# Kernel optimization log

Hardware: AMD Instinct MI355X
Metric: run time of the kernel (lower is better)

Reference implementation:

```python
import jax, jax.numpy as jnp
import numpy as np

B, L, D = 8, 512, 128
SCALE = float(np.sqrt(D))


def setup_inputs() -> dict:
    key = jax.random.key(0)
    ks = jax.random.split(key, 12)
    s = 1.0 / np.sqrt(D)
    inp = {
        "query": jax.random.normal(ks[0], (B, L, D), jnp.float32),
        "key": jax.random.normal(ks[1], (B, L, D), jnp.float32),
        "value": jax.random.normal(ks[2], (B, L, D), jnp.float32),
        # nn.Linear weights stored torch-style as (out, in); y = x @ W.T + b
        "Wq": jax.random.uniform(ks[3], (D, D), jnp.float32, -s, s),
        "bq": jax.random.uniform(ks[4], (D,), jnp.float32, -s, s),
        "Wk": jax.random.uniform(ks[5], (D, D), jnp.float32, -s, s),
        "bk": jax.random.uniform(ks[6], (D,), jnp.float32, -s, s),
        "Wv": jax.random.uniform(ks[7], (D, D), jnp.float32, -s, s),
        "bv": jax.random.uniform(ks[8], (D,), jnp.float32, -s, s),
        "w_delta": jax.random.uniform(ks[9], (D,), jnp.float32, -s, s),
        "b_delta": jnp.zeros((), jnp.float32),
        "w_sigma": jax.random.uniform(ks[10], (D,), jnp.float32, -s, s),
        "b_sigma": jnp.zeros((), jnp.float32),
        "w_theta": jax.random.uniform(ks[11], (D,), jnp.float32, -s, s),
        "b_theta": jnp.zeros((), jnp.float32),
    }
    return inp


def reference(query, key, value, Wq, bq, Wk, bk, Wv, bv,
              w_delta, b_delta, w_sigma, b_sigma, w_theta, b_theta):
    Q = query @ Wq.T + bq          # [B,Lq,D]
    K = key @ Wk.T + bk            # [B,Lk,D]
    V = value @ Wv.T + bv          # [B,Lk,D]
    e = jnp.tanh(Q[:, :, None, :] + K[:, None, :, :])  # [B,Lq,Lk,D]
    # base (sum/scale) + three linear score heads fuse into one reduction over D
    w_all = 1.0 / SCALE + w_delta + w_sigma + w_theta   # [D]
    b_all = b_delta + b_sigma + b_theta
    combined = jnp.einsum('bqkd,d->bqk', e, w_all) + b_all
    attn = jax.nn.softmax(combined, axis=-1)            # dropout in eval mode: identity
    out = jnp.einsum('bqk,bkd->bqd', attn, V)
    return out
```

## Files before the change

kernel.cpp:

```cpp
#include <hip/hip_runtime.h>


#define BB 8
#define LL 512
#define DD 128
#define NROW (BB*LL)
#define MATN (NROW*DD)
#define KSPLIT 8

static constexpr float C1 = 2.8853900817779268f;
static constexpr float LOG2E = 1.4426950408889634f;
static constexpr float INV_SCALE = 0.08838834764831845f;

typedef float v2f __attribute__((ext_vector_type(2)));

__device__ __forceinline__ float fast_exp2(float x) { return __builtin_amdgcn_exp2f(x); }
__device__ __forceinline__ float fast_rcp(float x)  { return __builtin_amdgcn_rcpf(x); }

__device__ __forceinline__ v2f mk2(float a, float b) { v2f r; r.x = a; r.y = b; return r; }

__device__ __forceinline__ v2f fma2(v2f a, v2f b, v2f c) {
#if __has_builtin(__builtin_elementwise_fma)
    return __builtin_elementwise_fma(a, b, c);
#else
    v2f r; r.x = fmaf(a.x, b.x, c.x); r.y = fmaf(a.y, b.y, c.y); return r;
#endif
}

__device__ __forceinline__ int dperm(int c) {
    const int pmap[4] = {0, 2, 1, 3};
    return (c & ~3) | pmap[c & 3];
}

__global__ __launch_bounds__(256) void proj_kernel(
    const float* __restrict__ query, const float* __restrict__ key,
    const float* __restrict__ value,
    const float* __restrict__ Wq, const float* __restrict__ bq,
    const float* __restrict__ Wk, const float* __restrict__ bk,
    const float* __restrict__ Wv, const float* __restrict__ bv,
    const float* __restrict__ wd, const float* __restrict__ wsg,
    const float* __restrict__ wtt, float* __restrict__ ws)
{
    __shared__ __align__(16) float Wl[128 * 66];
    __shared__ __align__(16) float Xl[32 * 66];

    const int bx = blockIdx.x;
    const int m  = bx >> 7;
    const int r0 = (bx & 127) * 32;
    const float* X    = (m == 0) ? query : (m == 1) ? key : value;
    const float* W    = (m == 0) ? Wq    : (m == 1) ? Wk  : Wv;
    const float* bias = (m == 0) ? bq    : (m == 1) ? bk  : bv;
    const int t = threadIdx.x;

    if (bx == 0 && t < 128) {
        ws[(size_t)3 * MATN + dperm(t)] =
            -2.0f * LOG2E * (INV_SCALE + wd[t] + wsg[t] + wtt[t]);
    }

    const int cg = t & 31;
    const int rg = t >> 5;

    v2f acc[4][4];
    #pragma unroll
    for (int j = 0; j < 4; ++j) {
        float bj = bias[cg + 32 * j];
        #pragma unroll
        for (int i = 0; i < 4; ++i) acc[i][j] = mk2(bj, 0.f);
    }

    const float4* Wsrc = (const float4*)W;
    const float4* Xsrc = (const float4*)X;

    for (int h = 0; h < 2; ++h) {
        __syncthreads();
        #pragma unroll
        for (int j = 0; j < 8; ++j) {
            int g = t + j * 256;
            int c = g >> 4, f4 = g & 15;
            float4 v = Wsrc[c * 32 + h * 16 + f4];
            float* dst = &Wl[c * 66 + f4 * 4];
            *(float2*)dst       = make_float2(v.x, v.y);
            *(float2*)(dst + 2) = make_float2(v.z, v.w);
        }
        #pragma unroll
        for (int j = 0; j < 2; ++j) {
            int g = t + j * 256;
            int r = g >> 4, f4 = g & 15;
            float4 v = Xsrc[(r0 + r) * 32 + h * 16 + f4];
            float* dst = &Xl[r * 66 + f4 * 4];
            *(float2*)dst       = make_float2(v.x, v.y);
            *(float2*)(dst + 2) = make_float2(v.z, v.w);
        }
        __syncthreads();

        #pragma unroll 4
        for (int dg = 0; dg < 32; ++dg) {
            v2f bf[4];
            #pragma unroll
            for (int j = 0; j < 4; ++j)
                bf[j] = *(const v2f*)&Wl[(cg + 32 * j) * 66 + 2 * dg];
            v2f af[4];
            #pragma unroll
            for (int i = 0; i < 4; ++i)
                af[i] = *(const v2f*)&Xl[(rg * 4 + i) * 66 + 2 * dg];
            #pragma unroll
            for (int i = 0; i < 4; ++i)
                #pragma unroll
                for (int j = 0; j < 4; ++j)
                    acc[i][j] = fma2(af[i], bf[j], acc[i][j]);
        }
    }

    if (m == 2) {
        float* oV = ws + (size_t)2 * MATN;
        #pragma unroll
        for (int i = 0; i < 4; ++i) {
            int r = r0 + rg * 4 + i;
            #pragma unroll
            for (int j = 0; j < 4; ++j)
                oV[(size_t)r * DD + cg + 32 * j] = acc[i][j].x + acc[i][j].y;
        }
    } else {
        float* oE = ws + (size_t)m * MATN;
        const int cp = dperm(cg);
        #pragma unroll
        for (int i = 0; i < 4; ++i) {
            int r = r0 + rg * 4 + i;
            #pragma unroll
            for (int j = 0; j < 4; ++j)
                oE[(size_t)r * DD + cp + 32 * j] =
                    fast_exp2(C1 * (acc[i][j].x + acc[i][j].y));
        }
    }
}

template <bool ATOMIC>
__global__ __launch_bounds__(512, 6) void attn_kernel(
    const float* __restrict__ ws, float* __restrict__ outp,
    float* __restrict__ psump)
{
    __shared__ __align__(16) float Ekt[64 * 132];
    __shared__ __align__(16) float wl[128];
    __shared__ __align__(16) float EqL[8 * 512];

    const float* Eq  = ws;
    const float* Ek  = ws + (size_t)MATN;
    const float* Vp  = ws + (size_t)2 * MATN;

    const int bx   = blockIdx.x;
    const int qblk = bx >> 3;
    const int kx   = bx & 7;
    const int b    = qblk >> 4;
    const int wave = __builtin_amdgcn_readfirstlane((int)threadIdx.x >> 6);
    const int lane = threadIdx.x & 63;
    const int qa   = qblk * 32 + wave * 4;
    const int eqo  = wave * 512;

    {
        const float4* EqW = (const float4*)(Eq + (size_t)qa * DD);
        float4 ea = EqW[2 * lane];
        float4 eb = EqW[2 * lane + 1];
        *(float4*)&EqL[eqo + 8 * lane]     = ea;
        *(float4*)&EqL[eqo + 8 * lane + 4] = eb;
    }

    {
        const float4* sK = (const float4*)(Ek + (size_t)b * (LL * DD)
                                              + (size_t)kx * 64 * DD);
        #pragma unroll
        for (int r = 0; r < 4; ++r) {
            int g = (int)threadIdx.x + r * 512;
            int row = g >> 5, c4 = g & 31;
            *(float4*)&Ekt[row * 132 + c4 * 4] = sK[g];
        }
        if (threadIdx.x < 32)
            ((float4*)wl)[threadIdx.x] =
                ((const float4*)(ws + (size_t)3 * MATN))[threadIdx.x];
    }
    __syncthreads();

    const float* krow = &Ekt[lane * 132];
    const float4* wl4 = (const float4*)wl;
    const float* eqp  = &EqL[eqo];
    v2f S0 = mk2(0.f, 0.f), S1 = S0, S2 = S0, S3 = S0;

    #pragma unroll 2
    for (int ih = 0; ih < 16; ++ih) {
        float4 K0 = *(const float4*)(krow + 8 * ih);
        float4 K1 = *(const float4*)(krow + 8 * ih + 4);
        float4 W0 = wl4[2 * ih];
        float4 W1 = wl4[2 * ih + 1];
        v2f k0lo = mk2(K0.x, K0.y), k0hi = mk2(K0.z, K0.w);
        v2f k1lo = mk2(K1.x, K1.y), k1hi = mk2(K1.z, K1.w);
        v2f w0lo = mk2(W0.x, W0.y), w0hi = mk2(W0.z, W0.w);
        v2f w1lo = mk2(W1.x, W1.y), w1hi = mk2(W1.z, W1.w);
        #define QT(SS, QQ) { \
            float4 A0 = *(const float4*)(eqp + (QQ) * 128 + 8 * ih); \
            float4 A1 = *(const float4*)(eqp + (QQ) * 128 + 8 * ih + 4); \
            v2f X  = fma2(mk2(A0.x, A0.y), k0lo, mk2(1.f, 1.f)); \
            v2f Y  = fma2(mk2(A0.z, A0.w), k0hi, mk2(1.f, 1.f)); \
            v2f D  = X * Y;                        \
            v2f N  = fma2(w0lo, Y, w0hi * X);      \
            v2f NU = N * mk2(D.y, D.x); \
            float rr = fast_rcp(D.x * D.y); \
            SS = fma2(NU, mk2(rr, rr), SS); \
            v2f X1  = fma2(mk2(A1.x, A1.y), k1lo, mk2(1.f, 1.f)); \
            v2f Y1  = fma2(mk2(A1.z, A1.w), k1hi, mk2(1.f, 1.f)); \
            v2f D1  = X1 * Y1; \
            v2f N1  = fma2(w1lo, Y1, w1hi * X1); \
            v2f NU1 = N1 * mk2(D1.y, D1.x); \
            float rr1 = fast_rcp(D1.x * D1.y); \
            SS = fma2(NU1, mk2(rr1, rr1), SS); }
        QT(S0, 0) QT(S1, 1) QT(S2, 2) QT(S3, 3)
        #undef QT
    }
    float p0 = fast_exp2(S0.x + S0.y);
    float p1 = fast_exp2(S1.x + S1.y);
    float p2 = fast_exp2(S2.x + S2.y);
    float p3 = fast_exp2(S3.x + S3.y);

    float t0 = p0, t1 = p1, t2 = p2, t3 = p3;
    #pragma unroll
    for (int off = 32; off; off >>= 1) {
        t0 += __shfl_xor(t0, off);
        t1 += __shfl_xor(t1, off);
        t2 += __shfl_xor(t2, off);
        t3 += __shfl_xor(t3, off);
    }
    if (lane == 0) {
        if (ATOMIC) {
            atomicAdd(&psump[qa + 0], t0);
            atomicAdd(&psump[qa + 1], t1);
            atomicAdd(&psump[qa + 2], t2);
            atomicAdd(&psump[qa + 3], t3);
        } else {
            float* pp = psump + (size_t)kx * NROW + qa;
            pp[0] = t0; pp[1] = t1; pp[2] = t2; pp[3] = t3;
        }
    }

    *(float4*)&EqL[eqo + 4 * lane] = make_float4(p0, p1, p2, p3);

    const v2f* __restrict__ Vg =
        (const v2f*)(Vp + (size_t)b * (LL * DD) + (size_t)kx * 64 * DD);
    v2f o[4];
    #pragma unroll
    for (int qq = 0; qq < 4; ++qq) o[qq] = mk2(0.f, 0.f);

    #pragma unroll
    for (int g = 0; g < 8; ++g) {
        v2f v[8];
        #pragma unroll
        for (int e = 0; e < 8; ++e)
            v[e] = Vg[(size_t)(8 * g + e) * 64 + lane];
        #pragma unroll
        for (int e = 0; e < 8; ++e) {
            int kidx = 8 * g + e;
            float4 pw = *(const float4*)&EqL[eqo + 4 * kidx];
            o[0] = fma2(mk2(pw.x, pw.x), v[e], o[0]);
            o[1] = fma2(mk2(pw.y, pw.y), v[e], o[1]);
            o[2] = fma2(mk2(pw.z, pw.z), v[e], o[2]);
            o[3] = fma2(mk2(pw.w, pw.w), v[e], o[3]);
        }
    }

    const int d2 = 2 * lane;
    if (ATOMIC) {
        #pragma unroll
        for (int qq = 0; qq < 4; ++qq) {
            atomicAdd(&outp[(size_t)(qa + qq) * DD + d2],     o[qq].x);
            atomicAdd(&outp[(size_t)(qa + qq) * DD + d2 + 1], o[qq].y);
        }
    } else {
        float* base = outp + (size_t)kx * MATN;
        #pragma unroll
        for (int qq = 0; qq < 4; ++qq)
            *(v2f*)&base[(size_t)(qa + qq) * DD + d2] = o[qq];
    }
}

__global__ __launch_bounds__(256) void reduce_kernel(
    const float* __restrict__ part, const float* __restrict__ psumP,
    float* __restrict__ out)
{
    int t = blockIdx.x * 256 + threadIdx.x;
    const float4* p4 = (const float4*)part;
    float4 acc = make_float4(0.f, 0.f, 0.f, 0.f);
    #pragma unroll
    for (int kx = 0; kx < KSPLIT; ++kx) {
        float4 v = p4[(size_t)kx * (MATN / 4) + t];
        acc.x += v.x; acc.y += v.y; acc.z += v.z; acc.w += v.w;
    }
    int q = t >> 5;
    float s = 0.f;
    #pragma unroll
    for (int kx = 0; kx < KSPLIT; ++kx) s += psumP[(size_t)kx * NROW + q];
    float inv = fast_rcp(s);
    ((float4*)out)[t] = make_float4(acc.x * inv, acc.y * inv,
                                    acc.z * inv, acc.w * inv);
}

__global__ __launch_bounds__(256) void norm_kernel(
    float* __restrict__ out, const float* __restrict__ psumG)
{
    int t = blockIdx.x * 256 + threadIdx.x;
    float2* o2 = (float2*)out;
    int q = t >> 6;
    float inv = fast_rcp(psumG[q]);
    float2 v = o2[t];
    o2[t] = make_float2(v.x * inv, v.y * inv);
}

extern "C" void kernel_launch(void* const* d_in, const int* in_sizes, int n_in,
                              void* d_out, int out_size, void* d_ws, size_t ws_size,
                              hipStream_t stream) {
    const float* query = (const float*)d_in[0];
    const float* key_  = (const float*)d_in[1];
    const float* value = (const float*)d_in[2];
    const float* Wq    = (const float*)d_in[3];
    const float* bq    = (const float*)d_in[4];
    const float* Wk    = (const float*)d_in[5];
    const float* bk    = (const float*)d_in[6];
    const float* Wv    = (const float*)d_in[7];
    const float* bv    = (const float*)d_in[8];
    const float* wd    = (const float*)d_in[9];
    const float* wsg   = (const float*)d_in[11];
    const float* wtt   = (const float*)d_in[13];
    float* ws = (float*)d_ws;
    float* out = (float*)d_out;

    const size_t off_psum = (size_t)3 * MATN + 128;
    const size_t off_part = off_psum + (size_t)KSPLIT * NROW;
    const size_t need = (off_part + (size_t)KSPLIT * MATN) * sizeof(float);

    proj_kernel<<<384, 256, 0, stream>>>(query, key_, value,
                                         Wq, bq, Wk, bk, Wv, bv,
                                         wd, wsg, wtt, ws);
    if (ws_size >= need) {
        float* psumP = ws + off_psum;
        float* part  = ws + off_part;
        attn_kernel<false><<<1024, 512, 0, stream>>>(ws, part, psumP);
        reduce_kernel<<<512, 256, 0, stream>>>(part, psumP, out);
    } else {
        float* psumG = ws + off_psum;
        hipMemsetAsync(out, 0, (size_t)out_size * sizeof(float), stream);
        hipMemsetAsync(psumG, 0, (size_t)NROW * sizeof(float), stream);
        attn_kernel<true><<<1024, 512, 0, stream>>>(ws, out, psumG);
        norm_kernel<<<1024, 256, 0, stream>>>(out, psumG);
    }
}
```

Before: 132.9 us.

## Double queries per wave in attention kernel and prefetch second projection half

```diff
diff --git a/kernel.cpp b/kernel.cpp
--- a/kernel.cpp
+++ b/kernel.cpp
@@ -71,44 +71,94 @@
     const float4* Wsrc = (const float4*)W;
     const float4* Xsrc = (const float4*)X;
 
-    for (int h = 0; h < 2; ++h) {
-        __syncthreads();
-        #pragma unroll
-        for (int j = 0; j < 8; ++j) {
-            int g = t + j * 256;
-            int c = g >> 4, f4 = g & 15;
-            float4 v = Wsrc[c * 32 + h * 16 + f4];
-            float* dst = &Wl[c * 66 + f4 * 4];
-            *(float2*)dst       = make_float2(v.x, v.y);
-            *(float2*)(dst + 2) = make_float2(v.z, v.w);
-        }
-        #pragma unroll
-        for (int j = 0; j < 2; ++j) {
-            int g = t + j * 256;
-            int r = g >> 4, f4 = g & 15;
-            float4 v = Xsrc[(r0 + r) * 32 + h * 16 + f4];
-            float* dst = &Xl[r * 66 + f4 * 4];
-            *(float2*)dst       = make_float2(v.x, v.y);
-            *(float2*)(dst + 2) = make_float2(v.z, v.w);
-        }
-        __syncthreads();
-
-        #pragma unroll 4
-        for (int dg = 0; dg < 32; ++dg) {
-            v2f bf[4];
+    #pragma unroll
+    for (int j = 0; j < 8; ++j) {
+        int g = t + j * 256;
+        int c = g >> 4, f4 = g & 15;
+        float4 v = Wsrc[c * 32 + f4];
+        float* dst = &Wl[c * 66 + f4 * 4];
+        *(float2*)dst       = make_float2(v.x, v.y);
+        *(float2*)(dst + 2) = make_float2(v.z, v.w);
+    }
+    #pragma unroll
+    for (int j = 0; j < 2; ++j) {
+        int g = t + j * 256;
+        int r = g >> 4, f4 = g & 15;
+        float4 v = Xsrc[(r0 + r) * 32 + f4];
+        float* dst = &Xl[r * 66 + f4 * 4];
+        *(float2*)dst       = make_float2(v.x, v.y);
+        *(float2*)(dst + 2) = make_float2(v.z, v.w);
+    }
+
+    float4 wp[8], xp[2];
+    #pragma unroll
+    for (int j = 0; j < 8; ++j) {
+        int g = t + j * 256;
+        int c = g >> 4, f4 = g & 15;
+        wp[j] = Wsrc[c * 32 + 16 + f4];
+    }
+    #pragma unroll
+    for (int j = 0; j < 2; ++j) {
+        int g = t + j * 256;
+        int r = g >> 4, f4 = g & 15;
+        xp[j] = Xsrc[(r0 + r) * 32 + 16 + f4];
+    }
+
+    __syncthreads();
+
+    #pragma unroll 4
+    for (int dg = 0; dg < 32; ++dg) {
+        v2f bf[4];
+        #pragma unroll
+        for (int j = 0; j < 4; ++j)
+            bf[j] = *(const v2f*)&Wl[(cg + 32 * j) * 66 + 2 * dg];
+        v2f af[4];
+        #pragma unroll
+        for (int i = 0; i < 4; ++i)
+            af[i] = *(const v2f*)&Xl[(rg * 4 + i) * 66 + 2 * dg];
+        #pragma unroll
+        for (int i = 0; i < 4; ++i)
             #pragma unroll
             for (int j = 0; j < 4; ++j)
-                bf[j] = *(const v2f*)&Wl[(cg + 32 * j) * 66 + 2 * dg];
-            v2f af[4];
+                acc[i][j] = fma2(af[i], bf[j], acc[i][j]);
+    }
+
+    __syncthreads();
+
+    #pragma unroll
+    for (int j = 0; j < 8; ++j) {
+        int g = t + j * 256;
+        int c = g >> 4, f4 = g & 15;
+        float* dst = &Wl[c * 66 + f4 * 4];
+        *(float2*)dst       = make_float2(wp[j].x, wp[j].y);
+        *(float2*)(dst + 2) = make_float2(wp[j].z, wp[j].w);
+    }
+    #pragma unroll
+    for (int j = 0; j < 2; ++j) {
+        int g = t + j * 256;
+        int r = g >> 4, f4 = g & 15;
+        float* dst = &Xl[r * 66 + f4 * 4];
+        *(float2*)dst       = make_float2(xp[j].x, xp[j].y);
+        *(float2*)(dst + 2) = make_float2(xp[j].z, xp[j].w);
+    }
+
+    __syncthreads();
+
+    #pragma unroll 4
+    for (int dg = 0; dg < 32; ++dg) {
+        v2f bf[4];
+        #pragma unroll
+        for (int j = 0; j < 4; ++j)
+            bf[j] = *(const v2f*)&Wl[(cg + 32 * j) * 66 + 2 * dg];
+        v2f af[4];
+        #pragma unroll
+        for (int i = 0; i < 4; ++i)
+            af[i] = *(const v2f*)&Xl[(rg * 4 + i) * 66 + 2 * dg];
+        #pragma unroll
+        for (int i = 0; i < 4; ++i)
             #pragma unroll
-            for (int i = 0; i < 4; ++i)
-                af[i] = *(const v2f*)&Xl[(rg * 4 + i) * 66 + 2 * dg];
-            #pragma unroll
-            for (int i = 0; i < 4; ++i)
-                #pragma unroll
-                for (int j = 0; j < 4; ++j)
-                    acc[i][j] = fma2(af[i], bf[j], acc[i][j]);
-        }
+            for (int j = 0; j < 4; ++j)
+                acc[i][j] = fma2(af[i], bf[j], acc[i][j]);
     }
 
     if (m == 2) {
@@ -135,13 +185,13 @@
 }
 
 template <bool ATOMIC>
-__global__ __launch_bounds__(512, 6) void attn_kernel(
+__global__ __launch_bounds__(512, 4) void attn_kernel(
     const float* __restrict__ ws, float* __restrict__ outp,
     float* __restrict__ psump)
 {
     __shared__ __align__(16) float Ekt[64 * 132];
     __shared__ __align__(16) float wl[128];
-    __shared__ __align__(16) float EqL[8 * 512];
+    __shared__ __align__(16) float EqL[8 * 1024];
 
     const float* Eq  = ws;
     const float* Ek  = ws + (size_t)MATN;
@@ -150,18 +200,19 @@
     const int bx   = blockIdx.x;
     const int qblk = bx >> 3;
     const int kx   = bx & 7;
-    const int b    = qblk >> 4;
+    const int b    = qblk >> 3;
     const int wave = __builtin_amdgcn_readfirstlane((int)threadIdx.x >> 6);
     const int lane = threadIdx.x & 63;
-    const int qa   = qblk * 32 + wave * 4;
-    const int eqo  = wave * 512;
+    const int qa   = qblk * 64 + wave * 8;
+    const int eqo  = wave * 1024;
 
     {
         const float4* EqW = (const float4*)(Eq + (size_t)qa * DD);
-        float4 ea = EqW[2 * lane];
-        float4 eb = EqW[2 * lane + 1];
-        *(float4*)&EqL[eqo + 8 * lane]     = ea;
-        *(float4*)&EqL[eqo + 8 * lane + 4] = eb;
+        #pragma unroll
+        for (int r = 0; r < 4; ++r) {
+            float4 e = EqW[lane + 64 * r];
+            *(float4*)&EqL[eqo + 4 * (lane + 64 * r)] = e;
+        }
     }
 
     {
@@ -182,7 +233,9 @@
     const float* krow = &Ekt[lane * 132];
     const float4* wl4 = (const float4*)wl;
     const float* eqp  = &EqL[eqo];
-    v2f S0 = mk2(0.f, 0.f), S1 = S0, S2 = S0, S3 = S0;
+    v2f S[8];
+    #pragma unroll
+    for (int qq = 0; qq < 8; ++qq) S[qq] = mk2(0.f, 0.f);
 
     #pragma unroll 2
     for (int ih = 0; ih < 16; ++ih) {
@@ -194,58 +247,60 @@
         v2f k1lo = mk2(K1.x, K1.y), k1hi = mk2(K1.z, K1.w);
         v2f w0lo = mk2(W0.x, W0.y), w0hi = mk2(W0.z, W0.w);
         v2f w1lo = mk2(W1.x, W1.y), w1hi = mk2(W1.z, W1.w);
-        #define QT(SS, QQ) { \
-            float4 A0 = *(const float4*)(eqp + (QQ) * 128 + 8 * ih); \
-            float4 A1 = *(const float4*)(eqp + (QQ) * 128 + 8 * ih + 4); \
-            v2f X  = fma2(mk2(A0.x, A0.y), k0lo, mk2(1.f, 1.f)); \
-            v2f Y  = fma2(mk2(A0.z, A0.w), k0hi, mk2(1.f, 1.f)); \
-            v2f D  = X * Y;                        \
-            v2f N  = fma2(w0lo, Y, w0hi * X);      \
-            v2f NU = N * mk2(D.y, D.x); \
-            float rr = fast_rcp(D.x * D.y); \
-            SS = fma2(NU, mk2(rr, rr), SS); \
-            v2f X1  = fma2(mk2(A1.x, A1.y), k1lo, mk2(1.f, 1.f)); \
-            v2f Y1  = fma2(mk2(A1.z, A1.w), k1hi, mk2(1.f, 1.f)); \
-            v2f D1  = X1 * Y1; \
-            v2f N1  = fma2(w1lo, Y1, w1hi * X1); \
-            v2f NU1 = N1 * mk2(D1.y, D1.x); \
-            float rr1 = fast_rcp(D1.x * D1.y); \
-            SS = fma2(NU1, mk2(rr1, rr1), SS); }
-        QT(S0, 0) QT(S1, 1) QT(S2, 2) QT(S3, 3)
-        #undef QT
-    }
-    float p0 = fast_exp2(S0.x + S0.y);
-    float p1 = fast_exp2(S1.x + S1.y);
-    float p2 = fast_exp2(S2.x + S2.y);
-    float p3 = fast_exp2(S3.x + S3.y);
-
-    float t0 = p0, t1 = p1, t2 = p2, t3 = p3;
-    #pragma unroll
-    for (int off = 32; off; off >>= 1) {
-        t0 += __shfl_xor(t0, off);
-        t1 += __shfl_xor(t1, off);
-        t2 += __shfl_xor(t2, off);
-        t3 += __shfl_xor(t3, off);
-    }
-    if (lane == 0) {
-        if (ATOMIC) {
-            atomicAdd(&psump[qa + 0], t0);
-            atomicAdd(&psump[qa + 1], t1);
-            atomicAdd(&psump[qa + 2], t2);
-            atomicAdd(&psump[qa + 3], t3);
-        } else {
-            float* pp = psump + (size_t)kx * NROW + qa;
-            pp[0] = t0; pp[1] = t1; pp[2] = t2; pp[3] = t3;
-        }
-    }
-
-    *(float4*)&EqL[eqo + 4 * lane] = make_float4(p0, p1, p2, p3);
+        #pragma unroll
+        for (int qq = 0; qq < 8; ++qq) {
+            float4 A0 = *(const float4*)(eqp + qq * 128 + 8 * ih);
+            float4 A1 = *(const float4*)(eqp + qq * 128 + 8 * ih + 4);
+            v2f X  = fma2(mk2(A0.x, A0.y), k0lo, mk2(1.f, 1.f));
+            v2f Y  = fma2(mk2(A0.z, A0.w), k0hi, mk2(1.f, 1.f));
+            v2f D  = X * Y;
+            v2f N  = fma2(w0lo, Y, w0hi * X);
+            v2f NU = N * mk2(D.y, D.x);
+            float rr = fast_rcp(D.x * D.y);
+            S[qq] = fma2(NU, mk2(rr, rr), S[qq]);
+            v2f X1  = fma2(mk2(A1.x, A1.y), k1lo, mk2(1.f, 1.f));
+            v2f Y1  = fma2(mk2(A1.z, A1.w), k1hi, mk2(1.f, 1.f));
+            v2f D1  = X1 * Y1;
+            v2f N1  = fma2(w1lo, Y1, w1hi * X1);
+            v2f NU1 = N1 * mk2(D1.y, D1.x);
+            float rr1 = fast_rcp(D1.x * D1.y);
+            S[qq] = fma2(NU1, mk2(rr1, rr1), S[qq]);
+        }
+    }
+    float p[8];
+    #pragma unroll
+    for (int qq = 0; qq < 8; ++qq) p[qq] = fast_exp2(S[qq].x + S[qq].y);
+
+    {
+        float tt[8];
+        #pragma unroll
+        for (int qq = 0; qq < 8; ++qq) tt[qq] = p[qq];
+        #pragma unroll
+        for (int off = 32; off; off >>= 1) {
+            #pragma unroll
+            for (int qq = 0; qq < 8; ++qq) tt[qq] += __shfl_xor(tt[qq], off);
+        }
+        if (lane == 0) {
+            if (ATOMIC) {
+                #pragma unroll
+                for (int qq = 0; qq < 8; ++qq)
+                    atomicAdd(&psump[qa + qq], tt[qq]);
+            } else {
+                float* pp = psump + (size_t)kx * NROW + qa;
+                #pragma unroll
+                for (int qq = 0; qq < 8; ++qq) pp[qq] = tt[qq];
+            }
+        }
+    }
+
+    *(float4*)&EqL[eqo + 8 * lane]     = make_float4(p[0], p[1], p[2], p[3]);
+    *(float4*)&EqL[eqo + 8 * lane + 4] = make_float4(p[4], p[5], p[6], p[7]);
 
     const v2f* __restrict__ Vg =
         (const v2f*)(Vp + (size_t)b * (LL * DD) + (size_t)kx * 64 * DD);
-    v2f o[4];
-    #pragma unroll
-    for (int qq = 0; qq < 4; ++qq) o[qq] = mk2(0.f, 0.f);
+    v2f o[8];
+    #pragma unroll
+    for (int qq = 0; qq < 8; ++qq) o[qq] = mk2(0.f, 0.f);
 
     #pragma unroll
     for (int g = 0; g < 8; ++g) {
@@ -256,25 +311,30 @@
         #pragma unroll
         for (int e = 0; e < 8; ++e) {
             int kidx = 8 * g + e;
-            float4 pw = *(const float4*)&EqL[eqo + 4 * kidx];
-            o[0] = fma2(mk2(pw.x, pw.x), v[e], o[0]);
-            o[1] = fma2(mk2(pw.y, pw.y), v[e], o[1]);
-            o[2] = fma2(mk2(pw.z, pw.z), v[e], o[2]);
-            o[3] = fma2(mk2(pw.w, pw.w), v[e], o[3]);
+            float4 pa = *(const float4*)&EqL[eqo + 8 * kidx];
+            float4 pb = *(const float4*)&EqL[eqo + 8 * kidx + 4];
+            o[0] = fma2(mk2(pa.x, pa.x), v[e], o[0]);
+            o[1] = fma2(mk2(pa.y, pa.y), v[e], o[1]);
+            o[2] = fma2(mk2(pa.z, pa.z), v[e], o[2]);
+            o[3] = fma2(mk2(pa.w, pa.w), v[e], o[3]);
+            o[4] = fma2(mk2(pb.x, pb.x), v[e], o[4]);
+            o[5] = fma2(mk2(pb.y, pb.y), v[e], o[5]);
+            o[6] = fma2(mk2(pb.z, pb.z), v[e], o[6]);
+            o[7] = fma2(mk2(pb.w, pb.w), v[e], o[7]);
         }
     }
 
     const int d2 = 2 * lane;
     if (ATOMIC) {
         #pragma unroll
-        for (int qq = 0; qq < 4; ++qq) {
+        for (int qq = 0; qq < 8; ++qq) {
             atomicAdd(&outp[(size_t)(qa + qq) * DD + d2],     o[qq].x);
             atomicAdd(&outp[(size_t)(qa + qq) * DD + d2 + 1], o[qq].y);
         }
     } else {
         float* base = outp + (size_t)kx * MATN;
         #pragma unroll
-        for (int qq = 0; qq < 4; ++qq)
+        for (int qq = 0; qq < 8; ++qq)
             *(v2f*)&base[(size_t)(qa + qq) * DD + d2] = o[qq];
     }
 }
@@ -339,13 +399,13 @@
     if (ws_size >= need) {
         float* psumP = ws + off_psum;
         float* part  = ws + off_part;
-        attn_kernel<false><<<1024, 512, 0, stream>>>(ws, part, psumP);
+        attn_kernel<false><<<512, 512, 0, stream>>>(ws, part, psumP);
         reduce_kernel<<<512, 256, 0, stream>>>(part, psumP, out);
     } else {
         float* psumG = ws + off_psum;
         hipMemsetAsync(out, 0, (size_t)out_size * sizeof(float), stream);
         hipMemsetAsync(psumG, 0, (size_t)NROW * sizeof(float), stream);
-        attn_kernel<true><<<1024, 512, 0, stream>>>(ws, out, psumG);
+        attn_kernel<true><<<512, 512, 0, stream>>>(ws, out, psumG);
         norm_kernel<<<1024, 256, 0, stream>>>(out, psumG);
     }
 }
```

Measured after the change: 134.0 us. No clear change (+0.8%).
